# Kernel optimization log

Measured on AMD Instinct MI355X. Metric: run time of the kernel, lower is better.

Reference implementation:

```python
import jax, jax.numpy as jnp
import numpy as np
from jax import lax


def _binarize(w):
    # XNOR-style sign binarization: sign(w) with sign(0) -> +1
    return jnp.where(w >= 0, 1.0, -1.0).astype(w.dtype)


def setup_inputs() -> dict:
    key = jax.random.key(0)
    kx, kw = jax.random.split(key)
    X = jax.random.normal(kx, (32, 256, 56, 56), dtype=jnp.float32)   # NCHW
    W = jax.random.normal(kw, (256, 256, 3, 3), dtype=jnp.float32)    # OIHW
    return {"X": X, "W": W}


def reference(X, W):
    Wb = _binarize(W)
    # F.conv2d default: padding=0 (VALID), stride=1
    out = lax.conv_general_dilated(
        X, Wb,
        window_strides=(1, 1),
        padding="VALID",
        dimension_numbers=("NCHW", "OIHW", "NCHW"),
    )
    return out  # [32, 256, 54, 54]
```

## Files before the change

### kernel.cpp

```cpp
#include <hip/hip_runtime.h>
#include <stdint.h>

typedef float f32x4 __attribute__((ext_vector_type(4)));
typedef __bf16 bf16x8 __attribute__((ext_vector_type(8)));
typedef unsigned short u16x8 __attribute__((ext_vector_type(8)));

#define NIMG 32
#define CIN  256
#define HWIN 3136
#define COUT 256
#define HWOUT 2916
#define NPOS 93312

#define XT_BYTES   ((size_t)NIMG*HWIN*CIN*2)
#define WT_OFF     (XT_BYTES + 8192)
#define WT_BYTES   ((size_t)36*2*128*64*2)
#define WS_NEED    (WT_OFF + WT_BYTES)

static __device__ __forceinline__ unsigned short f2bf(float f) {
    union { float f; uint32_t u; } v; v.f = f;
    return (unsigned short)((v.u + 0x7FFFu + ((v.u >> 16) & 1u)) >> 16);
}

static __device__ __forceinline__ void gload16(const void* g, void* l) {
    __builtin_amdgcn_global_load_lds(
        (const __attribute__((address_space(1))) void*)g,
        (__attribute__((address_space(3))) void*)l, 16, 0, 0);
}

static __device__ __forceinline__ uint32_t lds_a(const void* p) {
    return (uint32_t)(uintptr_t)(__attribute__((address_space(3))) const void*)p;
}

static __device__ __forceinline__ u16x8 ldsr(uint32_t addr) {
    u16x8 r;
    asm volatile("ds_read_b128 %0, %1" : "=v"(r) : "v"(addr));
    return r;
}

#define BAR()   __builtin_amdgcn_s_barrier()
#define LGKM0() do { asm volatile("s_waitcnt lgkmcnt(0)" ::: "memory"); \
                     __builtin_amdgcn_sched_barrier(0); } while (0)
#define VM8()   asm volatile("s_waitcnt vmcnt(8)" ::: "memory")
#define VM0()   asm volatile("s_waitcnt vmcnt(0)" ::: "memory")
#define PRIO1() __builtin_amdgcn_s_setprio(1)
#define PRIO0() __builtin_amdgcn_s_setprio(0)

#define MF(a_, b_, c_) __builtin_amdgcn_mfma_f32_16x16x32_bf16( \
    __builtin_bit_cast(bf16x8, a_), __builtin_bit_cast(bf16x8, b_), c_, 0, 0, 0)

#define M16()                                              \
    acc[0][0] = MF(a0, b0, acc[0][0]);                     \
    acc[1][0] = MF(a1, b0, acc[1][0]);                     \
    acc[2][0] = MF(a2, b0, acc[2][0]);                     \
    acc[3][0] = MF(a3, b0, acc[3][0]);                     \
    acc[0][1] = MF(a0, b1, acc[0][1]);                     \
    acc[1][1] = MF(a1, b1, acc[1][1]);                     \
    acc[2][1] = MF(a2, b1, acc[2][1]);                     \
    acc[3][1] = MF(a3, b1, acc[3][1]);                     \
    acc[0][2] = MF(a0, b2, acc[0][2]);                     \
    acc[1][2] = MF(a1, b2, acc[1][2]);                     \
    acc[2][2] = MF(a2, b2, acc[2][2]);                     \
    acc[3][2] = MF(a3, b2, acc[3][2]);                     \
    acc[0][3] = MF(a0, b3, acc[0][3]);                     \
    acc[1][3] = MF(a1, b3, acc[1][3]);                     \
    acc[2][3] = MF(a2, b3, acc[2][3]);                     \
    acc[3][3] = MF(a3, b3, acc[3][3]);

__global__ void wxform(const float* __restrict__ W, unsigned short* __restrict__ Wt) {
    int idx = blockIdx.x * 256 + threadIdx.x;
    int c6 = idx & 63;
    int o7 = (idx >> 6) & 127;
    int ob = (idx >> 13) & 1;
    int cc = (idx >> 14) & 3;
    int k9 = idx >> 16;
    int o = ob * 128 + o7;
    int c = cc * 64 + c6;
    float w = W[(size_t)(o * 256 + c) * 9 + k9];
    Wt[idx] = (w >= 0.0f) ? (unsigned short)0x3F80 : (unsigned short)0xBF80;
}

__global__ void xxform(const float* __restrict__ X, unsigned short* __restrict__ Xt) {
    __shared__ float tile[32][65];
    int bid = blockIdx.x;
    int hwc = bid % 49;
    int cc  = (bid / 49) & 7;
    int n   = bid / (49 * 8);
    int hw0 = hwc * 64;
    int c0  = cc * 32;
    int t = threadIdx.x;
    {
        int c = t >> 3;
        int w = (t & 7) * 8;
        const float* src = X + (size_t)(n * CIN + c0 + c) * HWIN + hw0 + w;
        float4 a = *(const float4*)src;
        float4 b = *(const float4*)(src + 4);
        tile[c][w + 0] = a.x; tile[c][w + 1] = a.y; tile[c][w + 2] = a.z; tile[c][w + 3] = a.w;
        tile[c][w + 4] = b.x; tile[c][w + 5] = b.y; tile[c][w + 6] = b.z; tile[c][w + 7] = b.w;
    }
    __syncthreads();
    {
        int w  = t >> 2;
        int cb = (t & 3) * 8;
        u16x8 v;
        #pragma unroll
        for (int j = 0; j < 8; ++j) v[j] = f2bf(tile[cb + j][w]);
        *(u16x8*)(Xt + (size_t)(n * HWIN + hw0 + w) * 256 + c0 + cb) = v;
    }
}

__global__ __launch_bounds__(256, 2)
void bconv_gemm(const unsigned short* __restrict__ Xt,
                const unsigned short* __restrict__ Wt,
                float* __restrict__ out) {
    __shared__ __align__(16) char smem[65536];

    const int t    = threadIdx.x;
    const int wid  = t >> 6;
    const int lane = t & 63;
    const int l15  = lane & 15;
    const int lg   = lane >> 4;
    const int wr   = wid >> 1;
    const int wc   = wid & 1;
    const int ob   = blockIdx.x;
    const uint32_t P0 = blockIdx.y * 128u;

    const uint32_t colxB = (uint32_t)(((t & 7) ^ ((t >> 3) & 7)) << 4);
    const uint32_t rowt  = (uint32_t)(t >> 3);

    const char* pA0 = (const char*)Wt + (size_t)ob * 16384 + rowt * 128 + colxB;

    const char* bB[4];
    #pragma unroll
    for (int r = 0; r < 4; ++r) {
        uint32_t pos = P0 + (uint32_t)(r * 32) + rowt;
        uint32_t ni = pos / (uint32_t)HWOUT;
        uint32_t rm = pos - ni * HWOUT;
        uint32_t ph = rm / 54u;
        uint32_t pw = rm - ph * 54u;
        bB[r] = (const char*)Xt + (size_t)(ni * HWIN + ph * 56u + pw) * 512 + colxB;
    }

    const uint32_t x7  = (uint32_t)(l15 & 7);
    const uint32_t ck0 = ((((uint32_t)lg) ^ x7) << 4);
    const uint32_t ck1 = (((4u | (uint32_t)lg) ^ x7) << 4);
    const uint32_t ar0 = (uint32_t)(wr * 64 + 0 * 16 + l15) * 128u;
    const uint32_t ar1 = (uint32_t)(wr * 64 + 1 * 16 + l15) * 128u;
    const uint32_t ar2 = (uint32_t)(wr * 64 + 2 * 16 + l15) * 128u;
    const uint32_t ar3 = (uint32_t)(wr * 64 + 3 * 16 + l15) * 128u;
    const uint32_t br0 = 16384u + (uint32_t)(wc * 64 + 0 * 16 + l15) * 128u;
    const uint32_t br1 = 16384u + (uint32_t)(wc * 64 + 1 * 16 + l15) * 128u;
    const uint32_t br2 = 16384u + (uint32_t)(wc * 64 + 2 * 16 + l15) * 128u;
    const uint32_t br3 = 16384u + (uint32_t)(wc * 64 + 3 * 16 + l15) * 128u;

    const uint32_t E = lds_a(smem);
    const uint32_t O = E + 32768u;

    f32x4 acc[4][4];
    #pragma unroll
    for (int m = 0; m < 4; ++m)
        #pragma unroll
        for (int n = 0; n < 4; ++n)
            acc[m][n] = (f32x4){0.f, 0.f, 0.f, 0.f};

    auto STAGE_A = [&](uint32_t bufoff, int kt) {
        const char* p = pA0 + (uint32_t)kt * 32768u;
        #pragma unroll
        for (int r = 0; r < 4; ++r)
            gload16(p + r * 4096, smem + bufoff + r * 4096 + (size_t)t * 16);
    };
    auto STAGE_B = [&](uint32_t bufoff, uint32_t koff) {
        #pragma unroll
        for (int r = 0; r < 4; ++r)
            gload16(bB[r] + koff, smem + bufoff + 16384 + r * 4096 + (size_t)t * 16);
    };

    uint32_t ccE = 2, k3E = 0, koffE = 256;
    uint32_t ccO = 3, k3O = 0, koffO = 384;
    auto adv2 = [](uint32_t& cc, uint32_t& k3, uint32_t& koff) {
        #pragma unroll
        for (int s = 0; s < 2; ++s) {
            if (cc == 3) { cc = 0; koff += ((k3 == 2) ? 54u : 1u) * 512u - 384u; k3 = (k3 == 2) ? 0u : k3 + 1u; }
            else         { cc++; koff += 128u; }
        }
    };

    STAGE_A(0, 0);      STAGE_B(0, 0);
    STAGE_A(32768u, 1); STAGE_B(32768u, 128);
    VM8();
    BAR();

    u16x8 a0, a1, a2, a3, b0, b1, b2, b3;

    auto ITER = [&](int kt, bool pf) {
        a0 = ldsr(E + ar0 + ck0); a1 = ldsr(E + ar1 + ck0);
        a2 = ldsr(E + ar2 + ck0); a3 = ldsr(E + ar3 + ck0);
        b0 = ldsr(E + br0 + ck0); b1 = ldsr(E + br1 + ck0);
        b2 = ldsr(E + br2 + ck0); b3 = ldsr(E + br3 + ck0);
        BAR(); LGKM0(); PRIO1();
        M16();
        PRIO0(); BAR();
        a0 = ldsr(E + ar0 + ck1); a1 = ldsr(E + ar1 + ck1);
        a2 = ldsr(E + ar2 + ck1); a3 = ldsr(E + ar3 + ck1);
        b0 = ldsr(E + br0 + ck1); b1 = ldsr(E + br1 + ck1);
        b2 = ldsr(E + br2 + ck1); b3 = ldsr(E + br3 + ck1);
        VM0();
        BAR(); LGKM0(); PRIO1();
        M16();
        PRIO0(); BAR();
        a0 = ldsr(O + ar0 + ck0); a1 = ldsr(O + ar1 + ck0);
        a2 = ldsr(O + ar2 + ck0); a3 = ldsr(O + ar3 + ck0);
        b0 = ldsr(O + br0 + ck0); b1 = ldsr(O + br1 + ck0);
        b2 = ldsr(O + br2 + ck0); b3 = ldsr(O + br3 + ck0);
        if (pf) { STAGE_A(0, kt + 2); STAGE_B(0, koffE); }
        BAR(); LGKM0(); PRIO1();
        M16();
        PRIO0(); BAR();
        a0 = ldsr(O + ar0 + ck1); a1 = ldsr(O + ar1 + ck1);
        a2 = ldsr(O + ar2 + ck1); a3 = ldsr(O + ar3 + ck1);
        b0 = ldsr(O + br0 + ck1); b1 = ldsr(O + br1 + ck1);
        b2 = ldsr(O + br2 + ck1); b3 = ldsr(O + br3 + ck1);
        if (pf) { STAGE_A(32768u, kt + 3); STAGE_B(32768u, koffO); VM8(); }
        else    { VM0(); }
        BAR(); LGKM0(); PRIO1();
        M16();
        PRIO0(); BAR();
        if (pf) { adv2(ccE, k3E, koffE); adv2(ccO, k3O, koffO); }
    };

    for (int kt = 0; kt < 34; kt += 2) ITER(kt, true);
    ITER(34, false);

    const int orow0 = ob * 128 + wr * 64;
    #pragma unroll
    for (int n = 0; n < 4; ++n) {
        uint32_t P = P0 + (uint32_t)(wc * 64 + n * 16 + l15);
        uint32_t ni = P / (uint32_t)HWOUT;
        uint32_t rm = P - ni * HWOUT;
        float* ob_ = out + (size_t)(ni * 256u + orow0) * HWOUT + rm;
        #pragma unroll
        for (int m = 0; m < 4; ++m)
            #pragma unroll
            for (int r = 0; r < 4; ++r)
                ob_[(size_t)(m * 16 + lg * 4 + r) * HWOUT] = acc[m][n][r];
    }
}

__global__ void bconv_fallback(const float* __restrict__ X, const float* __restrict__ W,
                               float* __restrict__ out) {
    size_t idx = (size_t)blockIdx.x * 256 + threadIdx.x;
    int ow = (int)(idx % 54);
    int oh = (int)((idx / 54) % 54);
    int o  = (int)((idx / 2916) % 256);
    int n  = (int)(idx / 746496);
    float s = 0.f;
    for (int c = 0; c < 256; ++c) {
        const float* xr = X + ((size_t)(n * 256 + c) * 56 + oh) * 56 + ow;
        const float* wr = W + (size_t)(o * 256 + c) * 9;
        #pragma unroll
        for (int kh = 0; kh < 3; ++kh)
            #pragma unroll
            for (int kw = 0; kw < 3; ++kw) {
                float w = wr[kh * 3 + kw];
                float x = xr[kh * 56 + kw];
                s += (w >= 0.f) ? x : -x;
            }
    }
    out[idx] = s;
}

extern "C" void kernel_launch(void* const* d_in, const int* in_sizes, int n_in,
                              void* d_out, int out_size, void* d_ws, size_t ws_size,
                              hipStream_t stream) {
    const float* X = (const float*)d_in[0];
    const float* W = (const float*)d_in[1];
    float* out = (float*)d_out;

    if (ws_size < WS_NEED) {
        bconv_fallback<<<93312, 256, 0, stream>>>(X, W, out);
        return;
    }
    unsigned short* Xt = (unsigned short*)d_ws;
    unsigned short* Wt = (unsigned short*)((char*)d_ws + WT_OFF);

    wxform<<<2304, 256, 0, stream>>>(W, Wt);
    xxform<<<12544, 256, 0, stream>>>(X, Xt);

    dim3 grid(2, 729);
    bconv_gemm<<<grid, 256, 0, stream>>>(Xt, Wt, out);
}
```

Before: 147.0 us.

## Software-pipeline LDS reads against MFMA clusters with double-buffered registers

Restructures the main loop so each k-step issues LDS reads for the next half-tile into a second register set while the MFMA cluster consumes the current set, cutting the barriers per step from eight to one. Global prefetch now targets the buffer just consumed, with a single counter instead of two. The weight transform index layout is also simplified. This raises register pressure and uses a full vmcnt(0) wait every step, which may expose global load latency.

Result: no change. 148.2 us (+0.8%).

```diff
diff --git a/kernel.cpp b/kernel.cpp
--- a/kernel.cpp
+++ b/kernel.cpp
@@ -14,7 +14,7 @@
 
 #define XT_BYTES   ((size_t)NIMG*HWIN*CIN*2)
 #define WT_OFF     (XT_BYTES + 8192)
-#define WT_BYTES   ((size_t)36*2*128*64*2)
+#define WT_BYTES   ((size_t)36*256*64*2)
 #define WS_NEED    (WT_OFF + WT_BYTES)
 
 static __device__ __forceinline__ unsigned short f2bf(float f) {
@@ -39,9 +39,8 @@
 }
 
 #define BAR()   __builtin_amdgcn_s_barrier()
-#define LGKM0() do { asm volatile("s_waitcnt lgkmcnt(0)" ::: "memory"); \
-                     __builtin_amdgcn_sched_barrier(0); } while (0)
-#define VM8()   asm volatile("s_waitcnt vmcnt(8)" ::: "memory")
+#define SCB()   __builtin_amdgcn_sched_barrier(0)
+#define LGKM0() do { asm volatile("s_waitcnt lgkmcnt(0)" ::: "memory"); SCB(); } while (0)
 #define VM0()   asm volatile("s_waitcnt vmcnt(0)" ::: "memory")
 #define PRIO1() __builtin_amdgcn_s_setprio(1)
 #define PRIO0() __builtin_amdgcn_s_setprio(0)
@@ -49,32 +48,30 @@
 #define MF(a_, b_, c_) __builtin_amdgcn_mfma_f32_16x16x32_bf16( \
     __builtin_bit_cast(bf16x8, a_), __builtin_bit_cast(bf16x8, b_), c_, 0, 0, 0)
 
-#define M16()                                              \
-    acc[0][0] = MF(a0, b0, acc[0][0]);                     \
-    acc[1][0] = MF(a1, b0, acc[1][0]);                     \
-    acc[2][0] = MF(a2, b0, acc[2][0]);                     \
-    acc[3][0] = MF(a3, b0, acc[3][0]);                     \
-    acc[0][1] = MF(a0, b1, acc[0][1]);                     \
-    acc[1][1] = MF(a1, b1, acc[1][1]);                     \
-    acc[2][1] = MF(a2, b1, acc[2][1]);                     \
-    acc[3][1] = MF(a3, b1, acc[3][1]);                     \
-    acc[0][2] = MF(a0, b2, acc[0][2]);                     \
-    acc[1][2] = MF(a1, b2, acc[1][2]);                     \
-    acc[2][2] = MF(a2, b2, acc[2][2]);                     \
-    acc[3][2] = MF(a3, b2, acc[3][2]);                     \
-    acc[0][3] = MF(a0, b3, acc[0][3]);                     \
-    acc[1][3] = MF(a1, b3, acc[1][3]);                     \
-    acc[2][3] = MF(a2, b3, acc[2][3]);                     \
-    acc[3][3] = MF(a3, b3, acc[3][3]);
+#define CLUSTER(A0_, A1_, A2_, A3_, B0_, B1_, B2_, B3_) do {                       \
+    acc[0][0]=MF(A0_,B0_,acc[0][0]); acc[1][0]=MF(A1_,B0_,acc[1][0]);              \
+    acc[2][0]=MF(A2_,B0_,acc[2][0]); acc[3][0]=MF(A3_,B0_,acc[3][0]);              \
+    acc[0][1]=MF(A0_,B1_,acc[0][1]); acc[1][1]=MF(A1_,B1_,acc[1][1]);              \
+    acc[2][1]=MF(A2_,B1_,acc[2][1]); acc[3][1]=MF(A3_,B1_,acc[3][1]);              \
+    acc[0][2]=MF(A0_,B2_,acc[0][2]); acc[1][2]=MF(A1_,B2_,acc[1][2]);              \
+    acc[2][2]=MF(A2_,B2_,acc[2][2]); acc[3][2]=MF(A3_,B2_,acc[3][2]);              \
+    acc[0][3]=MF(A0_,B3_,acc[0][3]); acc[1][3]=MF(A1_,B3_,acc[1][3]);              \
+    acc[2][3]=MF(A2_,B3_,acc[2][3]); acc[3][3]=MF(A3_,B3_,acc[3][3]);              \
+} while (0)
+
+#define RD8(A0_, A1_, A2_, A3_, B0_, B1_, B2_, B3_, base_, ck_) do {               \
+    A0_ = ldsr((base_) + ar0 + (ck_)); A1_ = ldsr((base_) + ar1 + (ck_));          \
+    A2_ = ldsr((base_) + ar2 + (ck_)); A3_ = ldsr((base_) + ar3 + (ck_));          \
+    B0_ = ldsr((base_) + br0 + (ck_)); B1_ = ldsr((base_) + br1 + (ck_));          \
+    B2_ = ldsr((base_) + br2 + (ck_)); B3_ = ldsr((base_) + br3 + (ck_));          \
+} while (0)
 
 __global__ void wxform(const float* __restrict__ W, unsigned short* __restrict__ Wt) {
     int idx = blockIdx.x * 256 + threadIdx.x;
     int c6 = idx & 63;
-    int o7 = (idx >> 6) & 127;
-    int ob = (idx >> 13) & 1;
+    int o  = (idx >> 6) & 255;
     int cc = (idx >> 14) & 3;
     int k9 = idx >> 16;
-    int o = ob * 128 + o7;
     int c = cc * 64 + c6;
     float w = W[(size_t)(o * 256 + c) * 9 + k9];
     Wt[idx] = (w >= 0.0f) ? (unsigned short)0x3F80 : (unsigned short)0xBF80;
@@ -163,73 +160,61 @@
         for (int n = 0; n < 4; ++n)
             acc[m][n] = (f32x4){0.f, 0.f, 0.f, 0.f};
 
-    auto STAGE_A = [&](uint32_t bufoff, int kt) {
+    auto STAGE = [&](uint32_t off, int kt, uint32_t kof) {
         const char* p = pA0 + (uint32_t)kt * 32768u;
         #pragma unroll
         for (int r = 0; r < 4; ++r)
-            gload16(p + r * 4096, smem + bufoff + r * 4096 + (size_t)t * 16);
+            gload16(p + r * 4096, smem + off + r * 4096 + (size_t)t * 16);
+        #pragma unroll
+        for (int r = 0; r < 4; ++r)
+            gload16(bB[r] + kof, smem + off + 16384 + r * 4096 + (size_t)t * 16);
     };
-    auto STAGE_B = [&](uint32_t bufoff, uint32_t koff) {
-        #pragma unroll
-        for (int r = 0; r < 4; ++r)
-            gload16(bB[r] + koff, smem + bufoff + 16384 + r * 4096 + (size_t)t * 16);
-    };
-
-    uint32_t ccE = 2, k3E = 0, koffE = 256;
-    uint32_t ccO = 3, k3O = 0, koffO = 384;
-    auto adv2 = [](uint32_t& cc, uint32_t& k3, uint32_t& koff) {
-        #pragma unroll
-        for (int s = 0; s < 2; ++s) {
-            if (cc == 3) { cc = 0; koff += ((k3 == 2) ? 54u : 1u) * 512u - 384u; k3 = (k3 == 2) ? 0u : k3 + 1u; }
-            else         { cc++; koff += 128u; }
+
+    uint32_t cc2 = 2, k32 = 0, koff2 = 256;
+
+    STAGE(0u, 0, 0u);
+    STAGE(32768u, 1, 128u);
+    VM0();
+    BAR();
+    SCB();
+
+    u16x8 s0a0, s0a1, s0a2, s0a3, s0b0, s0b1, s0b2, s0b3;
+    u16x8 s1a0, s1a1, s1a2, s1a3, s1b0, s1b1, s1b2, s1b3;
+
+    RD8(s0a0, s0a1, s0a2, s0a3, s0b0, s0b1, s0b2, s0b3, E, ck0);
+    LGKM0();
+
+    for (int kt = 0; kt < 36; ++kt) {
+        const uint32_t cur = (kt & 1) ? O : E;
+        const uint32_t nxt = (kt & 1) ? E : O;
+
+        RD8(s1a0, s1a1, s1a2, s1a3, s1b0, s1b1, s1b2, s1b3, cur, ck1);
+        SCB();
+        PRIO1();
+        CLUSTER(s0a0, s0a1, s0a2, s0a3, s0b0, s0b1, s0b2, s0b3);
+        PRIO0();
+        LGKM0();
+        VM0();
+        BAR();
+        SCB();
+        if (kt < 34) {
+            STAGE(cur, kt + 2, koff2);
+            if (cc2 == 3) { cc2 = 0; koff2 += ((k32 == 2) ? 54u : 1u) * 512u - 384u; k32 = (k32 == 2) ? 0u : k32 + 1u; }
+            else          { cc2++; koff2 += 128u; }
         }
-    };
-
-    STAGE_A(0, 0);      STAGE_B(0, 0);
-    STAGE_A(32768u, 1); STAGE_B(32768u, 128);
-    VM8();
-    BAR();
-
-    u16x8 a0, a1, a2, a3, b0, b1, b2, b3;
-
-    auto ITER = [&](int kt, bool pf) {
-        a0 = ldsr(E + ar0 + ck0); a1 = ldsr(E + ar1 + ck0);
-        a2 = ldsr(E + ar2 + ck0); a3 = ldsr(E + ar3 + ck0);
-        b0 = ldsr(E + br0 + ck0); b1 = ldsr(E + br1 + ck0);
-        b2 = ldsr(E + br2 + ck0); b3 = ldsr(E + br3 + ck0);
-        BAR(); LGKM0(); PRIO1();
-        M16();
-        PRIO0(); BAR();
-        a0 = ldsr(E + ar0 + ck1); a1 = ldsr(E + ar1 + ck1);
-        a2 = ldsr(E + ar2 + ck1); a3 = ldsr(E + ar3 + ck1);
-        b0 = ldsr(E + br0 + ck1); b1 = ldsr(E + br1 + ck1);
-        b2 = ldsr(E + br2 + ck1); b3 = ldsr(E + br3 + ck1);
-        VM0();
-        BAR(); LGKM0(); PRIO1();
-        M16();
-        PRIO0(); BAR();
-        a0 = ldsr(O + ar0 + ck0); a1 = ldsr(O + ar1 + ck0);
-        a2 = ldsr(O + ar2 + ck0); a3 = ldsr(O + ar3 + ck0);
-        b0 = ldsr(O + br0 + ck0); b1 = ldsr(O + br1 + ck0);
-        b2 = ldsr(O + br2 + ck0); b3 = ldsr(O + br3 + ck0);
-        if (pf) { STAGE_A(0, kt + 2); STAGE_B(0, koffE); }
-        BAR(); LGKM0(); PRIO1();
-        M16();
-        PRIO0(); BAR();
-        a0 = ldsr(O + ar0 + ck1); a1 = ldsr(O + ar1 + ck1);
-        a2 = ldsr(O + ar2 + ck1); a3 = ldsr(O + ar3 + ck1);
-        b0 = ldsr(O + br0 + ck1); b1 = ldsr(O + br1 + ck1);
-        b2 = ldsr(O + br2 + ck1); b3 = ldsr(O + br3 + ck1);
-        if (pf) { STAGE_A(32768u, kt + 3); STAGE_B(32768u, koffO); VM8(); }
-        else    { VM0(); }
-        BAR(); LGKM0(); PRIO1();
-        M16();
-        PRIO0(); BAR();
-        if (pf) { adv2(ccE, k3E, koffE); adv2(ccO, k3O, koffO); }
-    };
-
-    for (int kt = 0; kt < 34; kt += 2) ITER(kt, true);
-    ITER(34, false);
+        if (kt < 35) {
+            RD8(s0a0, s0a1, s0a2, s0a3, s0b0, s0b1, s0b2, s0b3, nxt, ck0);
+            SCB();
+            PRIO1();
+            CLUSTER(s1a0, s1a1, s1a2, s1a3, s1b0, s1b1, s1b2, s1b3);
+            PRIO0();
+            LGKM0();
+        } else {
+            PRIO1();
+            CLUSTER(s1a0, s1a1, s1a2, s1a3, s1b0, s1b1, s1b2, s1b3);
+            PRIO0();
+        }
+    }
 
     const int orow0 = ob * 128 + wr * 64;
     #pragma unroll
```
